# Performance work log

Hardware: AMD Instinct MI355X
Metric: run time of the kernel (lower is better)

## Reference

```python
import jax, jax.numpy as jnp
import numpy as np

N = 50257   # vocab size
D = 128     # embedding_dim
B = 2048    # batch
C = 10      # context window size


def setup_inputs() -> dict:
    key = jax.random.key(0)
    ks = jax.random.split(key, 16)
    s = 0.02
    return {
        "x_batch": jax.random.randint(ks[0], (B,), 0, N),
        "context_words_batch": jax.random.randint(ks[1], (B, C), 0, N),
        "eps": jax.random.normal(ks[2], (B, D), dtype=jnp.float32),
        # learned parameters
        "inf_emb": jax.random.normal(ks[3], (N, D), dtype=jnp.float32) * s,
        "W_aff": jax.random.normal(ks[4], (D, 2 * D), dtype=jnp.float32) * s,
        "b_aff": jnp.zeros((D,), dtype=jnp.float32),
        "W_mu": jax.random.normal(ks[5], (D, D), dtype=jnp.float32) * s,
        "b_mu": jnp.zeros((D,), dtype=jnp.float32),
        "W_sig": jax.random.normal(ks[6], (D, D), dtype=jnp.float32) * s,
        "b_sig": jnp.zeros((D,), dtype=jnp.float32),
        "gen_sigma_emb": jax.random.normal(ks[7], (N, D), dtype=jnp.float32) * s,
        "W_gen": jax.random.normal(ks[8], (N, D), dtype=jnp.float32) * s,
        "b_gen": jnp.zeros((N,), dtype=jnp.float32),
    }


def reference(x_batch, context_words_batch, eps, inf_emb, W_aff, b_aff,
              W_mu, b_mu, W_sig, b_sig, gen_sigma_emb, W_gen, b_gen):
    # ---- inference network (vectorized over batch and context) ----
    center = inf_emb[x_batch]                    # [B, D]
    ctx = inf_emb[context_words_batch]           # [B, C, D]
    center_rep = jnp.broadcast_to(center[:, None, :], ctx.shape)  # [B, C, D]
    cat = jnp.concatenate([center_rep, ctx], axis=-1)             # [B, C, 2D]
    h = jax.nn.relu(jnp.einsum("bce,de->bcd", cat, W_aff) + b_aff)
    h_sum = h.sum(axis=1)                        # [B, D]
    inf_mu = h_sum @ W_mu.T + b_mu               # [B, D]
    inf_sigma = jax.nn.softplus(h_sum @ W_sig.T + b_sig)

    # ---- reparameterized sample ----
    z = inf_mu + eps * inf_sigma                 # [B, D]

    # ---- generative / reconstruction term ----
    logits = z @ W_gen.T + b_gen                 # [B, N] (dominant intermediate)
    logp = jax.nn.log_softmax(logits, axis=-1)
    recon = jnp.take_along_axis(logp, context_words_batch, axis=1).sum(-1)  # [B]

    # ---- KL term (faithful to original, incl. use of generative sigma) ----
    sigma = jax.nn.softplus(gen_sigma_emb[x_batch])  # [B, D]
    kl = (jnp.log(sigma / inf_sigma)
          + (inf_sigma ** 2 + (inf_mu - sigma) ** 2) / (2.0 * sigma ** 2)
          - 0.5).sum(-1)                        # [B]

    return (kl - recon).mean()
```

## Files before the change

### kernel.cpp

```cpp
#include <hip/hip_runtime.h>
#include <float.h>
#include <math.h>

#define NV 50257
#define D 128
#define B 2048
#define C 10

#define NVPAD 50272
#define NTILES (NVPAD / 16)
#define NSTREAM 128
#define NG4 (NVPAD * D / 4)
#define LOG2E 1.44269504088896f
#define SC1 0x7F7F7F7F

typedef __attribute__((ext_vector_type(8))) short short8;
typedef __attribute__((ext_vector_type(8))) int int8v;
typedef __attribute__((ext_vector_type(4))) float float4v;
typedef __attribute__((ext_vector_type(2))) float float2v;

__device__ __forceinline__ float softplus_f(float x) {
    return fmaxf(x, 0.f) + log1pf(expf(-fabsf(x)));
}

__device__ __forceinline__ short f2bf(float f) {
    unsigned u = __float_as_uint(f);
    unsigned r = (u + 0x7FFFu + ((u >> 16) & 1u)) >> 16;
    return (short)r;
}

__global__ __launch_bounds__(256) void k_pre(
    const float* __restrict__ waff, const float* __restrict__ wmu,
    const float* __restrict__ wsig, const float* __restrict__ b_gen,
    short* __restrict__ waff_o, short* __restrict__ wmu_o,
    short* __restrict__ wsig_o, float* __restrict__ bg2, float* __restrict__ out)
{
    const int j = blockIdx.x * 256 + threadIdx.x;
    if (j == 0) out[0] = 0.f;
    if (j < 16384) {
        const float4* src; short4* dst; int jj;
        if (j < 8192)       { src = (const float4*)waff; dst = (short4*)waff_o; jj = j; }
        else if (j < 12288) { src = (const float4*)wmu;  dst = (short4*)wmu_o;  jj = j - 8192; }
        else                { src = (const float4*)wsig; dst = (short4*)wsig_o; jj = j - 12288; }
        const float4 g = src[jj];
        short4 o;
        o.x = f2bf(g.x); o.y = f2bf(g.y); o.z = f2bf(g.z); o.w = f2bf(g.w);
        dst[jj] = o;
    } else {
        const int jj = j - 16384;
        if (jj < NVPAD / 4) {
            const int e0 = jj * 4;
            float4 o;
            o.x = (e0 + 0 < NV) ? b_gen[e0 + 0] * LOG2E : -INFINITY;
            o.y = (e0 + 1 < NV) ? b_gen[e0 + 1] * LOG2E : -INFINITY;
            o.z = (e0 + 2 < NV) ? b_gen[e0 + 2] * LOG2E : -INFINITY;
            o.w = (e0 + 3 < NV) ? b_gen[e0 + 3] * LOG2E : -INFINITY;
            ((float4*)bg2)[jj] = o;
        }
    }
}

#define CONVB 629
__global__ __launch_bounds__(640, 1) void k_main(
    const int* __restrict__ x_batch, const int* __restrict__ ctxw,
    const float* __restrict__ eps, const float* __restrict__ inf_emb,
    const short* __restrict__ waff_bf, const float* __restrict__ b_aff,
    const short* __restrict__ wmu_bf, const float* __restrict__ b_mu,
    const short* __restrict__ wsig_bf, const float* __restrict__ b_sig,
    const float* __restrict__ gen_sig_emb, const float* __restrict__ wg,
    unsigned char* __restrict__ w8,
    float* __restrict__ z_out, unsigned char* __restrict__ z8_out,
    float* __restrict__ kl_out)
{
    const int bid = blockIdx.x;
    const int t = threadIdx.x;

    __shared__ float us[16][132];
    __shared__ float hsp[5][16][132];
    __shared__ float kl_s[8][16];

    if (bid >= 128) {
        const int base = (bid - 128) * (640 * 4) + t;
        #pragma unroll
        for (int k = 0; k < 4; ++k) {
            const int i4 = base + k * 640;
            if (i4 < NG4) {
                const int e0 = i4 * 4;
                int pk = 0;
                if (e0 < NV * D) {
                    const float4 g = ((const float4*)wg)[i4];
                    pk = __builtin_amdgcn_cvt_pk_fp8_f32(g.x, g.y, 0, false);
                    pk = __builtin_amdgcn_cvt_pk_fp8_f32(g.z, g.w, pk, true);
                }
                ((int*)w8)[i4] = pk;
            }
        }
        return;
    }

    const int b0 = bid * 16;
    const int wv = t >> 6;
    const int lane = t & 63;
    const int col16 = lane & 15;
    const int quad = lane >> 4;
    const int brow = b0 + col16;

    const int widx = ctxw[brow * C + wv];
    short8 cx[4];
    #pragma unroll
    for (int ks = 0; ks < 4; ++ks) {
        const float* p = inf_emb + (size_t)widx * D + ks * 32 + quad * 8;
        const float4 g0 = *(const float4*)p;
        const float4 g1 = *(const float4*)(p + 4);
        short8 v;
        v[0] = f2bf(g0.x); v[1] = f2bf(g0.y); v[2] = f2bf(g0.z); v[3] = f2bf(g0.w);
        v[4] = f2bf(g1.x); v[5] = f2bf(g1.y); v[6] = f2bf(g1.z); v[7] = f2bf(g1.w);
        cx[ks] = v;
    }

    if (wv < 8) {
        const int cidx = x_batch[brow];
        short8 ce[4];
        #pragma unroll
        for (int ks = 0; ks < 4; ++ks) {
            const float* p = inf_emb + (size_t)cidx * D + ks * 32 + quad * 8;
            const float4 g0 = *(const float4*)p;
            const float4 g1 = *(const float4*)(p + 4);
            short8 v;
            v[0] = f2bf(g0.x); v[1] = f2bf(g0.y); v[2] = f2bf(g0.z); v[3] = f2bf(g0.w);
            v[4] = f2bf(g1.x); v[5] = f2bf(g1.y); v[6] = f2bf(g1.z); v[7] = f2bf(g1.w);
            ce[ks] = v;
        }
        float4v acc = {0.f, 0.f, 0.f, 0.f};
        #pragma unroll
        for (int ks = 0; ks < 4; ++ks) {
            const short8 bw = *(const short8*)(waff_bf + (wv * 16 + col16) * 256 + ks * 32 + quad * 8);
            acc = __builtin_amdgcn_mfma_f32_16x16x32_bf16(ce[ks], bw, acc, 0, 0, 0);
        }
        #pragma unroll
        for (int r = 0; r < 4; ++r)
            us[quad * 4 + r][wv * 16 + col16] = acc[r];
    }
    __syncthreads();

    float ba[8];
    #pragma unroll
    for (int dt = 0; dt < 8; ++dt) ba[dt] = b_aff[dt * 16 + col16];

    float4v H[8];
    #pragma unroll
    for (int dt = 0; dt < 8; ++dt) {
        float4v a = {0.f, 0.f, 0.f, 0.f};
        #pragma unroll
        for (int ks = 0; ks < 4; ++ks) {
            const short8 bw = *(const short8*)(waff_bf + (dt * 16 + col16) * 256 + 128 + ks * 32 + quad * 8);
            a = __builtin_amdgcn_mfma_f32_16x16x32_bf16(cx[ks], bw, a, 0, 0, 0);
        }
        #pragma unroll
        for (int r = 0; r < 4; ++r) {
            const float u = us[quad * 4 + r][dt * 16 + col16];
            H[dt][r] = fmaxf(u + a[r] + ba[dt], 0.f);
        }
    }

    if (wv < 5) {
        #pragma unroll
        for (int dt = 0; dt < 8; ++dt)
            #pragma unroll
            for (int r = 0; r < 4; ++r)
                hsp[wv][quad * 4 + r][dt * 16 + col16] = H[dt][r];
    }
    __syncthreads();
    if (wv >= 5) {
        #pragma unroll
        for (int dt = 0; dt < 8; ++dt)
            #pragma unroll
            for (int r = 0; r < 4; ++r)
                hsp[wv - 5][quad * 4 + r][dt * 16 + col16] += H[dt][r];
    }
    __syncthreads();

    if (wv < 8) {
        short8 ha[4];
        #pragma unroll
        for (int ks = 0; ks < 4; ++ks) {
            const int off = ks * 32 + quad * 8;
            float4 s0 = {0.f, 0.f, 0.f, 0.f}, s1 = {0.f, 0.f, 0.f, 0.f};
            #pragma unroll
            for (int w = 0; w < 5; ++w) {
                const float4 a0 = *(const float4*)&hsp[w][col16][off];
                const float4 a1 = *(const float4*)&hsp[w][col16][off + 4];
                s0.x += a0.x; s0.y += a0.y; s0.z += a0.z; s0.w += a0.w;
                s1.x += a1.x; s1.y += a1.y; s1.z += a1.z; s1.w += a1.w;
            }
            short8 v;
            v[0] = f2bf(s0.x); v[1] = f2bf(s0.y); v[2] = f2bf(s0.z); v[3] = f2bf(s0.w);
            v[4] = f2bf(s1.x); v[5] = f2bf(s1.y); v[6] = f2bf(s1.z); v[7] = f2bf(s1.w);
            ha[ks] = v;
        }

        int xb2[4];
        #pragma unroll
        for (int r = 0; r < 4; ++r) xb2[r] = x_batch[b0 + quad * 4 + r];

        const int nt = wv;
        float4v mu4 = {0.f, 0.f, 0.f, 0.f};
        float4v sg4 = {0.f, 0.f, 0.f, 0.f};
        #pragma unroll
        for (int ks = 0; ks < 4; ++ks) {
            const short8 bm = *(const short8*)(wmu_bf + (nt * 16 + col16) * 128 + ks * 32 + quad * 8);
            const short8 bs = *(const short8*)(wsig_bf + (nt * 16 + col16) * 128 + ks * 32 + quad * 8);
            mu4 = __builtin_amdgcn_mfma_f32_16x16x32_bf16(ha[ks], bm, mu4, 0, 0, 0);
            sg4 = __builtin_amdgcn_mfma_f32_16x16x32_bf16(ha[ks], bs, sg4, 0, 0, 0);
        }
        const int d = nt * 16 + col16;
        const float bmu = b_mu[d];
        const float bsg = b_sig[d];
        float klp[4];
        #pragma unroll
        for (int r = 0; r < 4; ++r) {
            const int b = b0 + quad * 4 + r;
            const float mu = mu4[r] + bmu;
            const float sg = sg4[r] + bsg;
            const float isig = softplus_f(sg);
            const float e = eps[b * D + d];
            const float zz = fmaf(e, isig, mu);
            z_out[b * D + d] = zz;
            const int pk = __builtin_amdgcn_cvt_pk_fp8_f32(zz * LOG2E, 0.f, 0, false);
            z8_out[b * D + d] = (unsigned char)(pk & 0xFF);
            const float gs = softplus_f(gen_sig_emb[(size_t)xb2[r] * D + d]);
            const float diff = mu - gs;
            klp[r] = logf(gs / isig) + (isig * isig + diff * diff) / (2.f * gs * gs) - 0.5f;
        }
        #pragma unroll
        for (int off = 1; off < 16; off <<= 1)
            #pragma unroll
            for (int r = 0; r < 4; ++r)
                klp[r] += __shfl_xor(klp[r], off, 64);
        if (col16 == 0) {
            #pragma unroll
            for (int r = 0; r < 4; ++r)
                kl_s[wv][quad * 4 + r] = klp[r];
        }
    }
    __syncthreads();
    if (t < 16) {
        float s = 0.f;
        #pragma unroll
        for (int w = 0; w < 8; ++w) s += kl_s[w][t];
        kl_out[b0 + t] = s;
    }
}

#define LOADT8(bf, g, T) { \
    const int v_ = (T) < NTILES; \
    const int tt_ = v_ ? (T) : 0; \
    bf = *(const int8v*)(w8 + (size_t)(tt_ * 16 + col16) * D + quad * 32); \
    g = v_ ? bg2t[tt_ * 16 + col16] : -INFINITY; }

#define COMP8(bf, g) { \
    _Pragma("unroll") \
    for (int rt = 0; rt < 4; ++rt) { \
        float4v c = {g, g, g, g}; \
        c = __builtin_amdgcn_mfma_scale_f32_16x16x128_f8f6f4( \
                afrag[rt], bf, c, 0, 0, 0, SC1, 0, SC1); \
        _Pragma("unroll") \
        for (int r = 0; r < 4; ++r) \
            sums[rt][r] += __builtin_amdgcn_exp2f(c[r]); \
    } }

__global__ __launch_bounds__(256) void k_lse_mfma(
    const unsigned char* __restrict__ z8, const unsigned char* __restrict__ w8,
    const float* __restrict__ bg2t, float* __restrict__ part_s)
{
    const int bid = blockIdx.x;
    const int s = bid & 127;
    const int x = bid >> 7;
    const int t = threadIdx.x;
    const int wv = t >> 6;
    const int lane = t & 63;
    const int col16 = lane & 15;
    const int quad = lane >> 4;
    const int rowbase = x * 256 + wv * 64;

    int8v afrag[4];
    #pragma unroll
    for (int rt = 0; rt < 4; ++rt)
        afrag[rt] = *(const int8v*)(z8 + (size_t)(rowbase + rt * 16 + col16) * D + quad * 32);

    float sums[4][4];
    #pragma unroll
    for (int rt = 0; rt < 4; ++rt)
        #pragma unroll
        for (int r = 0; r < 4; ++r) sums[rt][r] = 0.f;

    int8v bA, bB, bC, bD;
    float gA, gB, gC, gD;
    LOADT8(bA, gA, s);
    LOADT8(bB, gB, s + 128);
    LOADT8(bC, gC, s + 256);
    LOADT8(bD, gD, s + 384);
    #pragma unroll 1
    for (int j = 0; j < 20; j += 4) {
        COMP8(bA, gA); LOADT8(bA, gA, s + (j + 4) * 128);
        COMP8(bB, gB); LOADT8(bB, gB, s + (j + 5) * 128);
        COMP8(bC, gC); LOADT8(bC, gC, s + (j + 6) * 128);
        COMP8(bD, gD); LOADT8(bD, gD, s + (j + 7) * 128);
    }
    COMP8(bA, gA);
    COMP8(bB, gB); COMP8(bC, gC); COMP8(bD, gD);
    LOADT8(bA, gA, s + 24 * 128);
    COMP8(bA, gA);

    #pragma unroll
    for (int off = 1; off < 16; off <<= 1)
        #pragma unroll
        for (int rt = 0; rt < 4; ++rt)
            #pragma unroll
            for (int r = 0; r < 4; ++r)
                sums[rt][r] += __shfl_xor(sums[rt][r], off, 64);

    if (col16 == 0) {
        #pragma unroll
        for (int rt = 0; rt < 4; ++rt)
            #pragma unroll
            for (int r = 0; r < 4; ++r) {
                const int row = rowbase + rt * 16 + quad * 4 + r;
                part_s[row * NSTREAM + s] = sums[rt][r];
            }
    }
}

__global__ __launch_bounds__(256) void k_final(
    const float* __restrict__ z, const unsigned char* __restrict__ w8,
    const float* __restrict__ b_gen, const int* __restrict__ ctxw,
    const float* __restrict__ part_s, const float* __restrict__ kl,
    float* __restrict__ out)
{
    const int t = threadIdx.x;
    const int wv = t >> 6;
    const int lane = t & 63;
    __shared__ float red[4];

    float wsum = 0.f;
    #pragma unroll
    for (int rr = 0; rr < 2; ++rr) {
        const int b = blockIdx.x * 8 + wv * 2 + rr;

        int idxs[C];
        #pragma unroll
        for (int c = 0; c < C; ++c) idxs[c] = ctxw[b * C + c];
        unsigned short uw[C];
        #pragma unroll
        for (int c = 0; c < C; ++c)
            uw[c] = *(const unsigned short*)(w8 + (size_t)idxs[c] * D + lane * 2);
        float sum_bg = 0.f;
        #pragma unroll
        for (int c = 0; c < C; ++c) sum_bg += b_gen[idxs[c]];

        float sv = part_s[b * NSTREAM + lane] + part_s[b * NSTREAM + 64 + lane];
        const float z0 = z[b * D + lane * 2];
        const float z1 = z[b * D + lane * 2 + 1];

        float acc = 0.f;
        #pragma unroll
        for (int c = 0; c < C; ++c) {
            const float2v wf = __builtin_amdgcn_cvt_pk_f32_fp8((int)uw[c], false);
            acc = fmaf(z0, wf[0], acc);
            acc = fmaf(z1, wf[1], acc);
        }
        #pragma unroll
        for (int off = 32; off > 0; off >>= 1) {
            sv  += __shfl_xor(sv, off, 64);
            acc += __shfl_xor(acc, off, 64);
        }
        if (lane == 0) {
            const float lse = logf(sv);
            const float recon = acc + sum_bg - C * lse;
            wsum += kl[b] - recon;
        }
    }
    if (lane == 0) red[wv] = wsum;
    __syncthreads();
    if (t == 0) atomicAdd(out, (red[0] + red[1] + red[2] + red[3]) * (1.f / B));
}

extern "C" void kernel_launch(void* const* d_in, const int* in_sizes, int n_in,
                              void* d_out, int out_size, void* d_ws, size_t ws_size,
                              hipStream_t stream) {
    const int* x_batch = (const int*)d_in[0];
    const int* ctxw    = (const int*)d_in[1];
    const float* eps   = (const float*)d_in[2];
    const float* inf_emb = (const float*)d_in[3];
    const float* W_aff = (const float*)d_in[4];
    const float* b_aff = (const float*)d_in[5];
    const float* W_mu  = (const float*)d_in[6];
    const float* b_mu  = (const float*)d_in[7];
    const float* W_sig = (const float*)d_in[8];
    const float* b_sig = (const float*)d_in[9];
    const float* gen_sig = (const float*)d_in[10];
    const float* W_gen = (const float*)d_in[11];
    const float* b_gen = (const float*)d_in[12];
    float* out = (float*)d_out;

    char* ws = (char*)d_ws;
    float* z      = (float*)ws;   ws += (size_t)B * D * 4;
    float* part_s = (float*)ws;   ws += (size_t)B * NSTREAM * 4;
    float* kl     = (float*)ws;   ws += (size_t)B * 4;
    float* bg2    = (float*)ws;   ws += (size_t)NVPAD * 4;
    unsigned char* z8 = (unsigned char*)ws;  ws += (size_t)B * D;
    unsigned char* w8 = (unsigned char*)ws;  ws += (size_t)NVPAD * D;
    short* waff_bf = (short*)ws;  ws += (size_t)128 * 256 * 2;
    short* wmu_bf  = (short*)ws;  ws += (size_t)128 * 128 * 2;
    short* wsig_bf = (short*)ws;  ws += (size_t)128 * 128 * 2;

    const int pre_items = 16384 + NVPAD / 4;
    hipLaunchKernelGGL(k_pre, dim3((pre_items + 255) / 256), dim3(256), 0, stream,
                       W_aff, W_mu, W_sig, b_gen,
                       waff_bf, wmu_bf, wsig_bf, bg2, out);
    hipLaunchKernelGGL(k_main, dim3(128 + CONVB), dim3(640), 0, stream,
                       x_batch, ctxw, eps, inf_emb, waff_bf, b_aff, wmu_bf, b_mu,
                       wsig_bf, b_sig, gen_sig, W_gen, w8, z, z8, kl);
    hipLaunchKernelGGL(k_lse_mfma, dim3(8 * NSTREAM), dim3(256), 0, stream,
                       z8, w8, bg2, part_s);
    hipLaunchKernelGGL(k_final, dim3(B / 8), dim3(256), 0, stream,
                       z, w8, b_gen, ctxw, part_s, kl, out);
}
```

Measured before the change: 177.5 us.

## Move W_gen FP8 conversion into pre-kernel and prefetch eps/gen_sigma loads

```diff
diff --git a/kernel.cpp b/kernel.cpp
--- a/kernel.cpp
+++ b/kernel.cpp
@@ -29,13 +29,39 @@
     return (short)r;
 }
 
+#define PRE_B 114
+#define CONVB8 786
 __global__ __launch_bounds__(256) void k_pre(
     const float* __restrict__ waff, const float* __restrict__ wmu,
     const float* __restrict__ wsig, const float* __restrict__ b_gen,
+    const float* __restrict__ wg,
     short* __restrict__ waff_o, short* __restrict__ wmu_o,
-    short* __restrict__ wsig_o, float* __restrict__ bg2, float* __restrict__ out)
+    short* __restrict__ wsig_o, float* __restrict__ bg2,
+    unsigned char* __restrict__ w8, float* __restrict__ out)
 {
-    const int j = blockIdx.x * 256 + threadIdx.x;
+    const int bid = blockIdx.x;
+    const int t = threadIdx.x;
+
+    if (bid >= PRE_B) {
+        const int base = (bid - PRE_B) * (256 * 8) + t;
+        #pragma unroll
+        for (int k = 0; k < 8; ++k) {
+            const int i4 = base + k * 256;
+            if (i4 < NG4) {
+                const int e0 = i4 * 4;
+                int pk = 0;
+                if (e0 < NV * D) {
+                    const float4 g = ((const float4*)wg)[i4];
+                    pk = __builtin_amdgcn_cvt_pk_fp8_f32(g.x, g.y, 0, false);
+                    pk = __builtin_amdgcn_cvt_pk_fp8_f32(g.z, g.w, pk, true);
+                }
+                ((int*)w8)[i4] = pk;
+            }
+        }
+        return;
+    }
+
+    const int j = bid * 256 + t;
     if (j == 0) out[0] = 0.f;
     if (j < 16384) {
         const float4* src; short4* dst; int jj;
@@ -60,15 +86,13 @@
     }
 }
 
-#define CONVB 629
 __global__ __launch_bounds__(640, 1) void k_main(
     const int* __restrict__ x_batch, const int* __restrict__ ctxw,
     const float* __restrict__ eps, const float* __restrict__ inf_emb,
     const short* __restrict__ waff_bf, const float* __restrict__ b_aff,
     const short* __restrict__ wmu_bf, const float* __restrict__ b_mu,
     const short* __restrict__ wsig_bf, const float* __restrict__ b_sig,
-    const float* __restrict__ gen_sig_emb, const float* __restrict__ wg,
-    unsigned char* __restrict__ w8,
+    const float* __restrict__ gen_sig_emb,
     float* __restrict__ z_out, unsigned char* __restrict__ z8_out,
     float* __restrict__ kl_out)
 {
@@ -78,25 +102,6 @@
     __shared__ float us[16][132];
     __shared__ float hsp[5][16][132];
     __shared__ float kl_s[8][16];
-
-    if (bid >= 128) {
-        const int base = (bid - 128) * (640 * 4) + t;
-        #pragma unroll
-        for (int k = 0; k < 4; ++k) {
-            const int i4 = base + k * 640;
-            if (i4 < NG4) {
-                const int e0 = i4 * 4;
-                int pk = 0;
-                if (e0 < NV * D) {
-                    const float4 g = ((const float4*)wg)[i4];
-                    pk = __builtin_amdgcn_cvt_pk_fp8_f32(g.x, g.y, 0, false);
-                    pk = __builtin_amdgcn_cvt_pk_fp8_f32(g.z, g.w, pk, true);
-                }
-                ((int*)w8)[i4] = pk;
-            }
-        }
-        return;
-    }
 
     const int b0 = bid * 16;
     const int wv = t >> 6;
@@ -116,6 +121,19 @@
         v[0] = f2bf(g0.x); v[1] = f2bf(g0.y); v[2] = f2bf(g0.z); v[3] = f2bf(g0.w);
         v[4] = f2bf(g1.x); v[5] = f2bf(g1.y); v[6] = f2bf(g1.z); v[7] = f2bf(g1.w);
         cx[ks] = v;
+    }
+
+    int xb2[4];
+    float gsr[4], epr[4];
+    const int dd = wv * 16 + col16;
+    if (wv < 8) {
+        #pragma unroll
+        for (int r = 0; r < 4; ++r) xb2[r] = x_batch[b0 + quad * 4 + r];
+        #pragma unroll
+        for (int r = 0; r < 4; ++r) {
+            gsr[r] = gen_sig_emb[(size_t)xb2[r] * D + dd];
+            epr[r] = eps[(b0 + quad * 4 + r) * D + dd];
+        }
     }
 
     if (wv < 8) {
@@ -199,10 +217,6 @@
             ha[ks] = v;
         }
 
-        int xb2[4];
-        #pragma unroll
-        for (int r = 0; r < 4; ++r) xb2[r] = x_batch[b0 + quad * 4 + r];
-
         const int nt = wv;
         float4v mu4 = {0.f, 0.f, 0.f, 0.f};
         float4v sg4 = {0.f, 0.f, 0.f, 0.f};
@@ -223,12 +237,12 @@
             const float mu = mu4[r] + bmu;
             const float sg = sg4[r] + bsg;
             const float isig = softplus_f(sg);
-            const float e = eps[b * D + d];
+            const float e = epr[r];
             const float zz = fmaf(e, isig, mu);
             z_out[b * D + d] = zz;
             const int pk = __builtin_amdgcn_cvt_pk_fp8_f32(zz * LOG2E, 0.f, 0, false);
             z8_out[b * D + d] = (unsigned char)(pk & 0xFF);
-            const float gs = softplus_f(gen_sig_emb[(size_t)xb2[r] * D + d]);
+            const float gs = softplus_f(gsr[r]);
             const float diff = mu - gs;
             klp[r] = logf(gs / isig) + (isig * isig + diff * diff) / (2.f * gs * gs) - 0.5f;
         }
@@ -414,13 +428,12 @@
     short* wmu_bf  = (short*)ws;  ws += (size_t)128 * 128 * 2;
     short* wsig_bf = (short*)ws;  ws += (size_t)128 * 128 * 2;
 
-    const int pre_items = 16384 + NVPAD / 4;
-    hipLaunchKernelGGL(k_pre, dim3((pre_items + 255) / 256), dim3(256), 0, stream,
-                       W_aff, W_mu, W_sig, b_gen,
-                       waff_bf, wmu_bf, wsig_bf, bg2, out);
-    hipLaunchKernelGGL(k_main, dim3(128 + CONVB), dim3(640), 0, stream,
+    hipLaunchKernelGGL(k_pre, dim3(PRE_B + CONVB8), dim3(256), 0, stream,
+                       W_aff, W_mu, W_sig, b_gen, W_gen,
+                       waff_bf, wmu_bf, wsig_bf, bg2, w8, out);
+    hipLaunchKernelGGL(k_main, dim3(128), dim3(640), 0, stream,
                        x_batch, ctxw, eps, inf_emb, waff_bf, b_aff, wmu_bf, b_mu,
-                       wsig_bf, b_sig, gen_sig, W_gen, w8, z, z8, kl);
+                       wsig_bf, b_sig, gen_sig, z, z8, kl);
     hipLaunchKernelGGL(k_lse_mfma, dim3(8 * NSTREAM), dim3(256), 0, stream,
                        z8, w8, bg2, part_s);
     hipLaunchKernelGGL(k_final, dim3(B / 8), dim3(256), 0, stream,
```

Result: slower. 182.1 us (+2.6%).

## Fuse all stages into one cooperative persistent kernel with grid syncs

Applied to the files above, without the earlier changes.

```diff
diff --git a/kernel.cpp b/kernel.cpp
--- a/kernel.cpp
+++ b/kernel.cpp
@@ -1,6 +1,9 @@
 #include <hip/hip_runtime.h>
+#include <hip/hip_cooperative_groups.h>
 #include <float.h>
 #include <math.h>
+
+namespace cg = cooperative_groups;
 
 #define NV 50257
 #define D 128
@@ -14,6 +17,9 @@
 #define LOG2E 1.44269504088896f
 #define SC1 0x7F7F7F7F
 
+#define MEGAB 512
+#define INFB 256
+
 typedef __attribute__((ext_vector_type(8))) short short8;
 typedef __attribute__((ext_vector_type(8))) int int8v;
 typedef __attribute__((ext_vector_type(4))) float float4v;
@@ -27,6 +33,369 @@
     unsigned u = __float_as_uint(f);
     unsigned r = (u + 0x7FFFu + ((u >> 16) & 1u)) >> 16;
     return (short)r;
+}
+
+#define LOADEMB(dst, idx) { \
+    const float* p_ = inf_emb + (size_t)(idx) * D; \
+    _Pragma("unroll") \
+    for (int ks_ = 0; ks_ < 4; ++ks_) { \
+        const float4 g0_ = *(const float4*)(p_ + ks_ * 32 + quad * 8); \
+        const float4 g1_ = *(const float4*)(p_ + ks_ * 32 + quad * 8 + 4); \
+        short8 v_; \
+        v_[0] = f2bf(g0_.x); v_[1] = f2bf(g0_.y); v_[2] = f2bf(g0_.z); v_[3] = f2bf(g0_.w); \
+        v_[4] = f2bf(g1_.x); v_[5] = f2bf(g1_.y); v_[6] = f2bf(g1_.z); v_[7] = f2bf(g1_.w); \
+        dst[ks_] = v_; } }
+
+#define ACCUM_H(cxf) { \
+    _Pragma("unroll") \
+    for (int dt_ = 0; dt_ < 8; ++dt_) { \
+        float4v a_ = {0.f, 0.f, 0.f, 0.f}; \
+        _Pragma("unroll") \
+        for (int ks_ = 0; ks_ < 4; ++ks_) { \
+            const short8 bw_ = *(const short8*)(waff_bf + (dt_ * 16 + col16) * 256 + 128 + ks_ * 32 + quad * 8); \
+            a_ = __builtin_amdgcn_mfma_f32_16x16x32_bf16(cxf[ks_], bw_, a_, 0, 0, 0); } \
+        _Pragma("unroll") \
+        for (int r_ = 0; r_ < 4; ++r_) { \
+            const float u_ = us[quad * 4 + r_][dt_ * 16 + col16]; \
+            H[dt_][r_] += fmaxf(u_ + a_[r_] + ba[dt_], 0.f); } } }
+
+#define LOADT8(bf, g, T) { \
+    const int v_ = (T) < NTILES; \
+    const int tt_ = v_ ? (T) : 0; \
+    bf = *(const int8v*)(w8 + (size_t)(tt_ * 16 + col16) * D + quad * 32); \
+    g = v_ ? bg2[tt_ * 16 + col16] : -INFINITY; }
+
+#define COMP8(bf, g) { \
+    _Pragma("unroll") \
+    for (int rt = 0; rt < 4; ++rt) { \
+        float4v c = {g, g, g, g}; \
+        c = __builtin_amdgcn_mfma_scale_f32_16x16x128_f8f6f4( \
+                afrag[rt], bf, c, 0, 0, 0, SC1, 0, SC1); \
+        _Pragma("unroll") \
+        for (int r = 0; r < 4; ++r) \
+            sums[rt][r] += __builtin_amdgcn_exp2f(c[r]); \
+    } }
+
+__global__ __launch_bounds__(256, 2) void k_mega(
+    const int* __restrict__ x_batch, const int* __restrict__ ctxw,
+    const float* __restrict__ eps, const float* __restrict__ inf_emb,
+    const float* __restrict__ W_aff, const float* __restrict__ b_aff,
+    const float* __restrict__ W_mu, const float* __restrict__ b_mu,
+    const float* __restrict__ W_sig, const float* __restrict__ b_sig,
+    const float* __restrict__ gen_sig_emb, const float* __restrict__ wg,
+    const float* __restrict__ b_gen,
+    short* __restrict__ waff_bf, short* __restrict__ wmu_bf, short* __restrict__ wsig_bf,
+    float* __restrict__ bg2, unsigned char* __restrict__ w8,
+    float* __restrict__ z_out, unsigned char* __restrict__ z8_out,
+    float* __restrict__ kl_out, float* __restrict__ part_s,
+    float* __restrict__ out)
+{
+    cg::grid_group grid = cg::this_grid();
+    const int bid = blockIdx.x;
+    const int t = threadIdx.x;
+    const int wv = t >> 6;
+    const int lane = t & 63;
+    const int col16 = lane & 15;
+    const int quad = lane >> 4;
+
+    __shared__ float us[16][132];
+    __shared__ float hsp[2][16][132];
+    __shared__ float kl_s[4][8];
+    __shared__ float red[4];
+
+    if (bid >= INFB) {
+        const int j = (bid - INFB) * 256 + t;
+        if (j == 0) out[0] = 0.f;
+        if (j < 16384) {
+            const float4* src; short4* dst; int jj;
+            if (j < 8192)       { src = (const float4*)W_aff; dst = (short4*)waff_bf; jj = j; }
+            else if (j < 12288) { src = (const float4*)W_mu;  dst = (short4*)wmu_bf;  jj = j - 8192; }
+            else                { src = (const float4*)W_sig; dst = (short4*)wsig_bf; jj = j - 12288; }
+            const float4 g = src[jj];
+            short4 o;
+            o.x = f2bf(g.x); o.y = f2bf(g.y); o.z = f2bf(g.z); o.w = f2bf(g.w);
+            dst[jj] = o;
+        } else {
+            const int jj = j - 16384;
+            if (jj < NVPAD / 4) {
+                const int e0 = jj * 4;
+                float4 o;
+                o.x = (e0 + 0 < NV) ? b_gen[e0 + 0] * LOG2E : -INFINITY;
+                o.y = (e0 + 1 < NV) ? b_gen[e0 + 1] * LOG2E : -INFINITY;
+                o.z = (e0 + 2 < NV) ? b_gen[e0 + 2] * LOG2E : -INFINITY;
+                o.w = (e0 + 3 < NV) ? b_gen[e0 + 3] * LOG2E : -INFINITY;
+                ((float4*)bg2)[jj] = o;
+            }
+        }
+    }
+    grid.sync();
+
+    if (bid < INFB) {
+        const int b0 = bid * 8;
+        const int brow = b0 + (col16 & 7);
+
+        const int nc = (wv < 2) ? 3 : 2;
+        const int wi0 = ctxw[brow * C + wv];
+        const int wi1 = ctxw[brow * C + wv + 4];
+        const int wi2 = (wv < 2) ? ctxw[brow * C + 8 + wv] : 0;
+        const int cidx = x_batch[brow];
+
+        short8 ce[4], cxa[4], cxb[4];
+        LOADEMB(ce, cidx);
+        LOADEMB(cxa, wi0);
+
+        float4v u0 = {0.f, 0.f, 0.f, 0.f}, u1 = {0.f, 0.f, 0.f, 0.f};
+        #pragma unroll
+        for (int ks = 0; ks < 4; ++ks) {
+            const short8 bw0 = *(const short8*)(waff_bf + ((wv    ) * 16 + col16) * 256 + ks * 32 + quad * 8);
+            const short8 bw1 = *(const short8*)(waff_bf + ((wv + 4) * 16 + col16) * 256 + ks * 32 + quad * 8);
+            u0 = __builtin_amdgcn_mfma_f32_16x16x32_bf16(ce[ks], bw0, u0, 0, 0, 0);
+            u1 = __builtin_amdgcn_mfma_f32_16x16x32_bf16(ce[ks], bw1, u1, 0, 0, 0);
+        }
+        #pragma unroll
+        for (int r = 0; r < 4; ++r) {
+            us[quad * 4 + r][(wv    ) * 16 + col16] = u0[r];
+            us[quad * 4 + r][(wv + 4) * 16 + col16] = u1[r];
+        }
+        __syncthreads();
+
+        float ba[8];
+        #pragma unroll
+        for (int dt = 0; dt < 8; ++dt) ba[dt] = b_aff[dt * 16 + col16];
+
+        float4v H[8];
+        #pragma unroll
+        for (int dt = 0; dt < 8; ++dt) H[dt] = (float4v){0.f, 0.f, 0.f, 0.f};
+
+        LOADEMB(cxb, wi1);
+        ACCUM_H(cxa);
+        if (nc == 3) {
+            LOADEMB(cxa, wi2);
+            ACCUM_H(cxb);
+            ACCUM_H(cxa);
+        } else {
+            ACCUM_H(cxb);
+        }
+
+        if (wv < 2) {
+            #pragma unroll
+            for (int dt = 0; dt < 8; ++dt)
+                #pragma unroll
+                for (int r = 0; r < 4; ++r)
+                    hsp[wv][quad * 4 + r][dt * 16 + col16] = H[dt][r];
+        }
+        __syncthreads();
+        if (wv >= 2) {
+            #pragma unroll
+            for (int dt = 0; dt < 8; ++dt)
+                #pragma unroll
+                for (int r = 0; r < 4; ++r)
+                    hsp[wv - 2][quad * 4 + r][dt * 16 + col16] += H[dt][r];
+        }
+        __syncthreads();
+
+        short8 ha[4];
+        #pragma unroll
+        for (int ks = 0; ks < 4; ++ks) {
+            const int off = ks * 32 + quad * 8;
+            const float4 a0 = *(const float4*)&hsp[0][col16][off];
+            const float4 b0v = *(const float4*)&hsp[1][col16][off];
+            const float4 a1 = *(const float4*)&hsp[0][col16][off + 4];
+            const float4 b1v = *(const float4*)&hsp[1][col16][off + 4];
+            short8 v;
+            v[0] = f2bf(a0.x + b0v.x); v[1] = f2bf(a0.y + b0v.y);
+            v[2] = f2bf(a0.z + b0v.z); v[3] = f2bf(a0.w + b0v.w);
+            v[4] = f2bf(a1.x + b1v.x); v[5] = f2bf(a1.y + b1v.y);
+            v[6] = f2bf(a1.z + b1v.z); v[7] = f2bf(a1.w + b1v.w);
+            ha[ks] = v;
+        }
+
+        const int d0 = wv * 16 + col16;
+        const int d1 = (wv + 4) * 16 + col16;
+        int xb2[4]; float gs0[4], gs1[4], ep0[4], ep1[4];
+        #pragma unroll
+        for (int r = 0; r < 4; ++r) {
+            const int br = b0 + ((quad * 4 + r) & 7);
+            xb2[r] = x_batch[br];
+            gs0[r] = gen_sig_emb[(size_t)xb2[r] * D + d0];
+            gs1[r] = gen_sig_emb[(size_t)xb2[r] * D + d1];
+            ep0[r] = eps[br * D + d0];
+            ep1[r] = eps[br * D + d1];
+        }
+
+        float4v mu0 = {0.f,0.f,0.f,0.f}, sg0v = {0.f,0.f,0.f,0.f};
+        float4v mu1 = {0.f,0.f,0.f,0.f}, sg1v = {0.f,0.f,0.f,0.f};
+        #pragma unroll
+        for (int ks = 0; ks < 4; ++ks) {
+            const short8 bm0 = *(const short8*)(wmu_bf  + ((wv    ) * 16 + col16) * 128 + ks * 32 + quad * 8);
+            const short8 bs0 = *(const short8*)(wsig_bf + ((wv    ) * 16 + col16) * 128 + ks * 32 + quad * 8);
+            const short8 bm1 = *(const short8*)(wmu_bf  + ((wv + 4) * 16 + col16) * 128 + ks * 32 + quad * 8);
+            const short8 bs1 = *(const short8*)(wsig_bf + ((wv + 4) * 16 + col16) * 128 + ks * 32 + quad * 8);
+            mu0  = __builtin_amdgcn_mfma_f32_16x16x32_bf16(ha[ks], bm0, mu0, 0, 0, 0);
+            sg0v = __builtin_amdgcn_mfma_f32_16x16x32_bf16(ha[ks], bs0, sg0v, 0, 0, 0);
+            mu1  = __builtin_amdgcn_mfma_f32_16x16x32_bf16(ha[ks], bm1, mu1, 0, 0, 0);
+            sg1v = __builtin_amdgcn_mfma_f32_16x16x32_bf16(ha[ks], bs1, sg1v, 0, 0, 0);
+        }
+
+        float klp[4] = {0.f, 0.f, 0.f, 0.f};
+        #pragma unroll
+        for (int half = 0; half < 2; ++half) {
+            const int d = half ? d1 : d0;
+            const float bmu = b_mu[d];
+            const float bsg = b_sig[d];
+            #pragma unroll
+            for (int r = 0; r < 4; ++r) {
+                const int b = b0 + quad * 4 + r;
+                const float mu = (half ? mu1[r] : mu0[r]) + bmu;
+                const float sg = (half ? sg1v[r] : sg0v[r]) + bsg;
+                const float isig = softplus_f(sg);
+                const float e = half ? ep1[r] : ep0[r];
+                const float zz = fmaf(e, isig, mu);
+                if (quad < 2) {
+                    z_out[b * D + d] = zz;
+                    const int pk = __builtin_amdgcn_cvt_pk_fp8_f32(zz * LOG2E, 0.f, 0, false);
+                    z8_out[b * D + d] = (unsigned char)(pk & 0xFF);
+                }
+                const float gs = softplus_f(half ? gs1[r] : gs0[r]);
+                const float diff = mu - gs;
+                klp[r] += logf(gs / isig) + (isig * isig + diff * diff) / (2.f * gs * gs) - 0.5f;
+            }
+        }
+        #pragma unroll
+        for (int off = 1; off < 16; off <<= 1)
+            #pragma unroll
+            for (int r = 0; r < 4; ++r)
+                klp[r] += __shfl_xor(klp[r], off, 64);
+        if (col16 == 0 && quad < 2) {
+            #pragma unroll
+            for (int r = 0; r < 4; ++r)
+                kl_s[wv][quad * 4 + r] = klp[r];
+        }
+        __syncthreads();
+        if (t < 8) {
+            float s = 0.f;
+            #pragma unroll
+            for (int w = 0; w < 4; ++w) s += kl_s[w][t];
+            kl_out[b0 + t] = s;
+        }
+    } else {
+        const int base = (bid - INFB) * 256 + t;
+        #pragma unroll 5
+        for (int k = 0; k < 25; ++k) {
+            const int i4 = base + k * 65536;
+            if (i4 < NG4) {
+                const int e0 = i4 * 4;
+                int pk = 0;
+                if (e0 < NV * D) {
+                    const float4 g = ((const float4*)wg)[i4];
+                    pk = __builtin_amdgcn_cvt_pk_fp8_f32(g.x, g.y, 0, false);
+                    pk = __builtin_amdgcn_cvt_pk_fp8_f32(g.z, g.w, pk, true);
+                }
+                ((int*)w8)[i4] = pk;
+            }
+        }
+    }
+    grid.sync();
+
+    #pragma unroll 1
+    for (int rep = 0; rep < 2; ++rep) {
+        const int gwid = bid * 4 + wv + rep * 2048;
+        const int s = gwid & 127;
+        const int x = gwid >> 7;
+        const int rowbase = x * 64;
+
+        int8v afrag[4];
+        #pragma unroll
+        for (int rt = 0; rt < 4; ++rt)
+            afrag[rt] = *(const int8v*)(z8_out + (size_t)(rowbase + rt * 16 + col16) * D + quad * 32);
+
+        float sums[4][4];
+        #pragma unroll
+        for (int rt = 0; rt < 4; ++rt)
+            #pragma unroll
+            for (int r = 0; r < 4; ++r) sums[rt][r] = 0.f;
+
+        int8v bA, bB, bC, bD;
+        float gA, gB, gC, gD;
+        LOADT8(bA, gA, s);
+        LOADT8(bB, gB, s + 128);
+        LOADT8(bC, gC, s + 256);
+        LOADT8(bD, gD, s + 384);
+        #pragma unroll 1
+        for (int j = 0; j < 20; j += 4) {
+            COMP8(bA, gA); LOADT8(bA, gA, s + (j + 4) * 128);
+            COMP8(bB, gB); LOADT8(bB, gB, s + (j + 5) * 128);
+            COMP8(bC, gC); LOADT8(bC, gC, s + (j + 6) * 128);
+            COMP8(bD, gD); LOADT8(bD, gD, s + (j + 7) * 128);
+        }
+        COMP8(bA, gA);
+        COMP8(bB, gB); COMP8(bC, gC); COMP8(bD, gD);
+        LOADT8(bA, gA, s + 24 * 128);
+        COMP8(bA, gA);
+
+        #pragma unroll
+        for (int off = 1; off < 16; off <<= 1)
+            #pragma unroll
+            for (int rt = 0; rt < 4; ++rt)
+                #pragma unroll
+                for (int r = 0; r < 4; ++r)
+                    sums[rt][r] += __shfl_xor(sums[rt][r], off, 64);
+
+        if (col16 == 0) {
+            #pragma unroll
+            for (int rt = 0; rt < 4; ++rt)
+                #pragma unroll
+                for (int r = 0; r < 4; ++r) {
+                    const int row = rowbase + rt * 16 + quad * 4 + r;
+                    part_s[row * NSTREAM + s] = sums[rt][r];
+                }
+        }
+    }
+    grid.sync();
+
+    if (bid < INFB) {
+        float wsum = 0.f;
+        #pragma unroll
+        for (int rr = 0; rr < 2; ++rr) {
+            const int b = bid * 8 + wv * 2 + rr;
+
+            int idxs[C];
+            #pragma unroll
+            for (int c = 0; c < C; ++c) idxs[c] = ctxw[b * C + c];
+            unsigned short uw[C];
+            #pragma unroll
+            for (int c = 0; c < C; ++c)
+                uw[c] = *(const unsigned short*)(w8 + (size_t)idxs[c] * D + lane * 2);
+            float sum_bg = 0.f;
+            #pragma unroll
+            for (int c = 0; c < C; ++c) sum_bg += b_gen[idxs[c]];
+
+            float sv = part_s[b * NSTREAM + lane] + part_s[b * NSTREAM + 64 + lane];
+            const float z0 = z_out[b * D + lane * 2];
+            const float z1 = z_out[b * D + lane * 2 + 1];
+
+            float acc = 0.f;
+            #pragma unroll
+            for (int c = 0; c < C; ++c) {
+                const float2v wf = __builtin_amdgcn_cvt_pk_f32_fp8((int)uw[c], false);
+                acc = fmaf(z0, wf[0], acc);
+                acc = fmaf(z1, wf[1], acc);
+            }
+            #pragma unroll
+            for (int off = 32; off > 0; off >>= 1) {
+                sv  += __shfl_xor(sv, off, 64);
+                acc += __shfl_xor(acc, off, 64);
+            }
+            if (lane == 0) {
+                const float lse = logf(sv);
+                const float recon = acc + sum_bg - C * lse;
+                wsum += kl_out[b] - recon;
+            }
+        }
+        if (lane == 0) red[wv] = wsum;
+        __syncthreads();
+        if (t == 0) atomicAdd(out, (red[0] + red[1] + red[2] + red[3]) * (1.f / B));
+    }
 }
 
 __global__ __launch_bounds__(256) void k_pre(
@@ -107,30 +476,12 @@
 
     const int widx = ctxw[brow * C + wv];
     short8 cx[4];
-    #pragma unroll
-    for (int ks = 0; ks < 4; ++ks) {
-        const float* p = inf_emb + (size_t)widx * D + ks * 32 + quad * 8;
-        const float4 g0 = *(const float4*)p;
-        const float4 g1 = *(const float4*)(p + 4);
-        short8 v;
-        v[0] = f2bf(g0.x); v[1] = f2bf(g0.y); v[2] = f2bf(g0.z); v[3] = f2bf(g0.w);
-        v[4] = f2bf(g1.x); v[5] = f2bf(g1.y); v[6] = f2bf(g1.z); v[7] = f2bf(g1.w);
-        cx[ks] = v;
-    }
+    LOADEMB(cx, widx);
 
     if (wv < 8) {
         const int cidx = x_batch[brow];
         short8 ce[4];
-        #pragma unroll
-        for (int ks = 0; ks < 4; ++ks) {
-            const float* p = inf_emb + (size_t)cidx * D + ks * 32 + quad * 8;
-            const float4 g0 = *(const float4*)p;
-            const float4 g1 = *(const float4*)(p + 4);
-            short8 v;
-            v[0] = f2bf(g0.x); v[1] = f2bf(g0.y); v[2] = f2bf(g0.z); v[3] = f2bf(g0.w);
-            v[4] = f2bf(g1.x); v[5] = f2bf(g1.y); v[6] = f2bf(g1.z); v[7] = f2bf(g1.w);
-            ce[ks] = v;
-        }
+        LOADEMB(ce, cidx);
         float4v acc = {0.f, 0.f, 0.f, 0.f};
         #pragma unroll
         for (int ks = 0; ks < 4; ++ks) {
@@ -252,26 +603,9 @@
     }
 }
 
-#define LOADT8(bf, g, T) { \
-    const int v_ = (T) < NTILES; \
-    const int tt_ = v_ ? (T) : 0; \
-    bf = *(const int8v*)(w8 + (size_t)(tt_ * 16 + col16) * D + quad * 32); \
-    g = v_ ? bg2t[tt_ * 16 + col16] : -INFINITY; }
-
-#define COMP8(bf, g) { \
-    _Pragma("unroll") \
-    for (int rt = 0; rt < 4; ++rt) { \
-        float4v c = {g, g, g, g}; \
-        c = __builtin_amdgcn_mfma_scale_f32_16x16x128_f8f6f4( \
-                afrag[rt], bf, c, 0, 0, 0, SC1, 0, SC1); \
-        _Pragma("unroll") \
-        for (int r = 0; r < 4; ++r) \
-            sums[rt][r] += __builtin_amdgcn_exp2f(c[r]); \
-    } }
-
 __global__ __launch_bounds__(256) void k_lse_mfma(
     const unsigned char* __restrict__ z8, const unsigned char* __restrict__ w8,
-    const float* __restrict__ bg2t, float* __restrict__ part_s)
+    const float* __restrict__ bg2, float* __restrict__ part_s)
 {
     const int bid = blockIdx.x;
     const int s = bid & 127;
@@ -414,15 +748,28 @@
     short* wmu_bf  = (short*)ws;  ws += (size_t)128 * 128 * 2;
     short* wsig_bf = (short*)ws;  ws += (size_t)128 * 128 * 2;
 
-    const int pre_items = 16384 + NVPAD / 4;
-    hipLaunchKernelGGL(k_pre, dim3((pre_items + 255) / 256), dim3(256), 0, stream,
-                       W_aff, W_mu, W_sig, b_gen,
-                       waff_bf, wmu_bf, wsig_bf, bg2, out);
-    hipLaunchKernelGGL(k_main, dim3(128 + CONVB), dim3(640), 0, stream,
-                       x_batch, ctxw, eps, inf_emb, waff_bf, b_aff, wmu_bf, b_mu,
-                       wsig_bf, b_sig, gen_sig, W_gen, w8, z, z8, kl);
-    hipLaunchKernelGGL(k_lse_mfma, dim3(8 * NSTREAM), dim3(256), 0, stream,
-                       z8, w8, bg2, part_s);
-    hipLaunchKernelGGL(k_final, dim3(B / 8), dim3(256), 0, stream,
-                       z, w8, b_gen, ctxw, part_s, kl, out);
+    void* kargs[] = {
+        (void*)&x_batch, (void*)&ctxw, (void*)&eps, (void*)&inf_emb,
+        (void*)&W_aff, (void*)&b_aff, (void*)&W_mu, (void*)&b_mu,
+        (void*)&W_sig, (void*)&b_sig, (void*)&gen_sig, (void*)&W_gen, (void*)&b_gen,
+        (void*)&waff_bf, (void*)&wmu_bf, (void*)&wsig_bf,
+        (void*)&bg2, (void*)&w8, (void*)&z, (void*)&z8, (void*)&kl, (void*)&part_s,
+        (void*)&out
+    };
+    hipError_t err = hipLaunchCooperativeKernel((const void*)k_mega, dim3(MEGAB), dim3(256),
+                                                kargs, 0, stream);
+    if (err != hipSuccess) {
+        (void)hipGetLastError();
+        const int pre_items = 16384 + NVPAD / 4;
+        hipLaunchKernelGGL(k_pre, dim3((pre_items + 255) / 256), dim3(256), 0, stream,
+                           W_aff, W_mu, W_sig, b_gen,
+                           waff_bf, wmu_bf, wsig_bf, bg2, out);
+        hipLaunchKernelGGL(k_main, dim3(128 + CONVB), dim3(640), 0, stream,
+                           x_batch, ctxw, eps, inf_emb, waff_bf, b_aff, wmu_bf, b_mu,
+                           wsig_bf, b_sig, gen_sig, W_gen, w8, z, z8, kl);
+        hipLaunchKernelGGL(k_lse_mfma, dim3(8 * NSTREAM), dim3(256), 0, stream,
+                           z8, w8, bg2, part_s);
+        hipLaunchKernelGGL(k_final, dim3(B / 8), dim3(256), 0, stream,
+                           z, w8, b_gen, ctxw, part_s, kl, out);
+    }
 }
```

Measured after the change: 370.6 us. 109% more time.

## Drop pre-kernel by converting weights inline and staging embedding gathers in LDS

Applied to the files above, without the earlier changes.

```diff
diff --git a/kernel.cpp b/kernel.cpp
--- a/kernel.cpp
+++ b/kernel.cpp
@@ -29,54 +29,36 @@
     return (short)r;
 }
 
-__global__ __launch_bounds__(256) void k_pre(
-    const float* __restrict__ waff, const float* __restrict__ wmu,
-    const float* __restrict__ wsig, const float* __restrict__ b_gen,
-    short* __restrict__ waff_o, short* __restrict__ wmu_o,
-    short* __restrict__ wsig_o, float* __restrict__ bg2, float* __restrict__ out)
-{
-    const int j = blockIdx.x * 256 + threadIdx.x;
-    if (j == 0) out[0] = 0.f;
-    if (j < 16384) {
-        const float4* src; short4* dst; int jj;
-        if (j < 8192)       { src = (const float4*)waff; dst = (short4*)waff_o; jj = j; }
-        else if (j < 12288) { src = (const float4*)wmu;  dst = (short4*)wmu_o;  jj = j - 8192; }
-        else                { src = (const float4*)wsig; dst = (short4*)wsig_o; jj = j - 12288; }
-        const float4 g = src[jj];
-        short4 o;
-        o.x = f2bf(g.x); o.y = f2bf(g.y); o.z = f2bf(g.z); o.w = f2bf(g.w);
-        dst[jj] = o;
-    } else {
-        const int jj = j - 16384;
-        if (jj < NVPAD / 4) {
-            const int e0 = jj * 4;
-            float4 o;
-            o.x = (e0 + 0 < NV) ? b_gen[e0 + 0] * LOG2E : -INFINITY;
-            o.y = (e0 + 1 < NV) ? b_gen[e0 + 1] * LOG2E : -INFINITY;
-            o.z = (e0 + 2 < NV) ? b_gen[e0 + 2] * LOG2E : -INFINITY;
-            o.w = (e0 + 3 < NV) ? b_gen[e0 + 3] * LOG2E : -INFINITY;
-            ((float4*)bg2)[jj] = o;
-        }
-    }
-}
+#define LOADW8(dst, base_ptr) { \
+    const float4 w0_ = *(const float4*)(base_ptr); \
+    const float4 w1_ = *(const float4*)((base_ptr) + 4); \
+    short8 v_; \
+    v_[0] = f2bf(w0_.x); v_[1] = f2bf(w0_.y); v_[2] = f2bf(w0_.z); v_[3] = f2bf(w0_.w); \
+    v_[4] = f2bf(w1_.x); v_[5] = f2bf(w1_.y); v_[6] = f2bf(w1_.z); v_[7] = f2bf(w1_.w); \
+    dst = v_; }
 
 #define CONVB 629
 __global__ __launch_bounds__(640, 1) void k_main(
     const int* __restrict__ x_batch, const int* __restrict__ ctxw,
     const float* __restrict__ eps, const float* __restrict__ inf_emb,
-    const short* __restrict__ waff_bf, const float* __restrict__ b_aff,
-    const short* __restrict__ wmu_bf, const float* __restrict__ b_mu,
-    const short* __restrict__ wsig_bf, const float* __restrict__ b_sig,
+    const float* __restrict__ W_aff, const float* __restrict__ b_aff,
+    const float* __restrict__ W_mu, const float* __restrict__ b_mu,
+    const float* __restrict__ W_sig, const float* __restrict__ b_sig,
     const float* __restrict__ gen_sig_emb, const float* __restrict__ wg,
-    unsigned char* __restrict__ w8,
+    const float* __restrict__ b_gen,
+    unsigned char* __restrict__ w8, float* __restrict__ bg2,
     float* __restrict__ z_out, unsigned char* __restrict__ z8_out,
     float* __restrict__ kl_out)
 {
     const int bid = blockIdx.x;
     const int t = threadIdx.x;
 
+    __shared__ union {
+        float hsp[5][16][132];
+        unsigned short rows[176][136];
+    } u;
+    __shared__ int idx_s[176];
     __shared__ float us[16][132];
-    __shared__ float hsp[5][16][132];
     __shared__ float kl_s[8][16];
 
     if (bid >= 128) {
@@ -95,6 +77,16 @@
                 ((int*)w8)[i4] = pk;
             }
         }
+        const int jb = (bid - 128) * 640 + t;
+        if (jb < NVPAD / 4) {
+            const int e0 = jb * 4;
+            float4 o;
+            o.x = (e0 + 0 < NV) ? b_gen[e0 + 0] * LOG2E : -INFINITY;
+            o.y = (e0 + 1 < NV) ? b_gen[e0 + 1] * LOG2E : -INFINITY;
+            o.z = (e0 + 2 < NV) ? b_gen[e0 + 2] * LOG2E : -INFINITY;
+            o.w = (e0 + 3 < NV) ? b_gen[e0 + 3] * LOG2E : -INFINITY;
+            ((float4*)bg2)[jb] = o;
+        }
         return;
     }
 
@@ -103,38 +95,38 @@
     const int lane = t & 63;
     const int col16 = lane & 15;
     const int quad = lane >> 4;
-    const int brow = b0 + col16;
-
-    const int widx = ctxw[brow * C + wv];
+
+    if (t < 160) {
+        idx_s[16 + (t % 10) * 16 + (t / 10)] = ctxw[b0 * C + t];
+    } else if (t < 176) {
+        idx_s[t - 160] = x_batch[b0 + (t - 160)];
+    }
+    __syncthreads();
+
+    for (int s = wv; s < 176; s += 10) {
+        const float2 g = ((const float2*)(inf_emb + (size_t)idx_s[s] * D))[lane];
+        ushort2 o;
+        o.x = (unsigned short)f2bf(g.x);
+        o.y = (unsigned short)f2bf(g.y);
+        *(ushort2*)&u.rows[s][lane * 2] = o;
+    }
+    __syncthreads();
+
     short8 cx[4];
     #pragma unroll
-    for (int ks = 0; ks < 4; ++ks) {
-        const float* p = inf_emb + (size_t)widx * D + ks * 32 + quad * 8;
-        const float4 g0 = *(const float4*)p;
-        const float4 g1 = *(const float4*)(p + 4);
-        short8 v;
-        v[0] = f2bf(g0.x); v[1] = f2bf(g0.y); v[2] = f2bf(g0.z); v[3] = f2bf(g0.w);
-        v[4] = f2bf(g1.x); v[5] = f2bf(g1.y); v[6] = f2bf(g1.z); v[7] = f2bf(g1.w);
-        cx[ks] = v;
-    }
+    for (int ks = 0; ks < 4; ++ks)
+        cx[ks] = *(const short8*)&u.rows[16 + wv * 16 + col16][ks * 32 + quad * 8];
 
     if (wv < 8) {
-        const int cidx = x_batch[brow];
         short8 ce[4];
         #pragma unroll
+        for (int ks = 0; ks < 4; ++ks)
+            ce[ks] = *(const short8*)&u.rows[col16][ks * 32 + quad * 8];
+        float4v acc = {0.f, 0.f, 0.f, 0.f};
+        #pragma unroll
         for (int ks = 0; ks < 4; ++ks) {
-            const float* p = inf_emb + (size_t)cidx * D + ks * 32 + quad * 8;
-            const float4 g0 = *(const float4*)p;
-            const float4 g1 = *(const float4*)(p + 4);
-            short8 v;
-            v[0] = f2bf(g0.x); v[1] = f2bf(g0.y); v[2] = f2bf(g0.z); v[3] = f2bf(g0.w);
-            v[4] = f2bf(g1.x); v[5] = f2bf(g1.y); v[6] = f2bf(g1.z); v[7] = f2bf(g1.w);
-            ce[ks] = v;
-        }
-        float4v acc = {0.f, 0.f, 0.f, 0.f};
-        #pragma unroll
-        for (int ks = 0; ks < 4; ++ks) {
-            const short8 bw = *(const short8*)(waff_bf + (wv * 16 + col16) * 256 + ks * 32 + quad * 8);
+            short8 bw;
+            LOADW8(bw, W_aff + (wv * 16 + col16) * 256 + ks * 32 + quad * 8);
             acc = __builtin_amdgcn_mfma_f32_16x16x32_bf16(ce[ks], bw, acc, 0, 0, 0);
         }
         #pragma unroll
@@ -153,13 +145,14 @@
         float4v a = {0.f, 0.f, 0.f, 0.f};
         #pragma unroll
         for (int ks = 0; ks < 4; ++ks) {
-            const short8 bw = *(const short8*)(waff_bf + (dt * 16 + col16) * 256 + 128 + ks * 32 + quad * 8);
+            short8 bw;
+            LOADW8(bw, W_aff + (dt * 16 + col16) * 256 + 128 + ks * 32 + quad * 8);
             a = __builtin_amdgcn_mfma_f32_16x16x32_bf16(cx[ks], bw, a, 0, 0, 0);
         }
         #pragma unroll
         for (int r = 0; r < 4; ++r) {
-            const float u = us[quad * 4 + r][dt * 16 + col16];
-            H[dt][r] = fmaxf(u + a[r] + ba[dt], 0.f);
+            const float uu = us[quad * 4 + r][dt * 16 + col16];
+            H[dt][r] = fmaxf(uu + a[r] + ba[dt], 0.f);
         }
     }
 
@@ -168,7 +161,7 @@
         for (int dt = 0; dt < 8; ++dt)
             #pragma unroll
             for (int r = 0; r < 4; ++r)
-                hsp[wv][quad * 4 + r][dt * 16 + col16] = H[dt][r];
+                u.hsp[wv][quad * 4 + r][dt * 16 + col16] = H[dt][r];
     }
     __syncthreads();
     if (wv >= 5) {
@@ -176,7 +169,7 @@
         for (int dt = 0; dt < 8; ++dt)
             #pragma unroll
             for (int r = 0; r < 4; ++r)
-                hsp[wv - 5][quad * 4 + r][dt * 16 + col16] += H[dt][r];
+                u.hsp[wv - 5][quad * 4 + r][dt * 16 + col16] += H[dt][r];
     }
     __syncthreads();
 
@@ -188,8 +181,8 @@
             float4 s0 = {0.f, 0.f, 0.f, 0.f}, s1 = {0.f, 0.f, 0.f, 0.f};
             #pragma unroll
             for (int w = 0; w < 5; ++w) {
-                const float4 a0 = *(const float4*)&hsp[w][col16][off];
-                const float4 a1 = *(const float4*)&hsp[w][col16][off + 4];
+                const float4 a0 = *(const float4*)&u.hsp[w][col16][off];
+                const float4 a1 = *(const float4*)&u.hsp[w][col16][off + 4];
                 s0.x += a0.x; s0.y += a0.y; s0.z += a0.z; s0.w += a0.w;
                 s1.x += a1.x; s1.y += a1.y; s1.z += a1.z; s1.w += a1.w;
             }
@@ -208,8 +201,9 @@
         float4v sg4 = {0.f, 0.f, 0.f, 0.f};
         #pragma unroll
         for (int ks = 0; ks < 4; ++ks) {
-            const short8 bm = *(const short8*)(wmu_bf + (nt * 16 + col16) * 128 + ks * 32 + quad * 8);
-            const short8 bs = *(const short8*)(wsig_bf + (nt * 16 + col16) * 128 + ks * 32 + quad * 8);
+            short8 bm, bs;
+            LOADW8(bm, W_mu  + (nt * 16 + col16) * 128 + ks * 32 + quad * 8);
+            LOADW8(bs, W_sig + (nt * 16 + col16) * 128 + ks * 32 + quad * 8);
             mu4 = __builtin_amdgcn_mfma_f32_16x16x32_bf16(ha[ks], bm, mu4, 0, 0, 0);
             sg4 = __builtin_amdgcn_mfma_f32_16x16x32_bf16(ha[ks], bs, sg4, 0, 0, 0);
         }
@@ -271,9 +265,11 @@
 
 __global__ __launch_bounds__(256) void k_lse_mfma(
     const unsigned char* __restrict__ z8, const unsigned char* __restrict__ w8,
-    const float* __restrict__ bg2t, float* __restrict__ part_s)
+    const float* __restrict__ bg2t, float* __restrict__ part_s,
+    float* __restrict__ out)
 {
     const int bid = blockIdx.x;
+    if (bid == 0 && threadIdx.x == 0) out[0] = 0.f;
     const int s = bid & 127;
     const int x = bid >> 7;
     const int t = threadIdx.x;
@@ -410,19 +406,12 @@
     float* bg2    = (float*)ws;   ws += (size_t)NVPAD * 4;
     unsigned char* z8 = (unsigned char*)ws;  ws += (size_t)B * D;
     unsigned char* w8 = (unsigned char*)ws;  ws += (size_t)NVPAD * D;
-    short* waff_bf = (short*)ws;  ws += (size_t)128 * 256 * 2;
-    short* wmu_bf  = (short*)ws;  ws += (size_t)128 * 128 * 2;
-    short* wsig_bf = (short*)ws;  ws += (size_t)128 * 128 * 2;
-
-    const int pre_items = 16384 + NVPAD / 4;
-    hipLaunchKernelGGL(k_pre, dim3((pre_items + 255) / 256), dim3(256), 0, stream,
-                       W_aff, W_mu, W_sig, b_gen,
-                       waff_bf, wmu_bf, wsig_bf, bg2, out);
+
     hipLaunchKernelGGL(k_main, dim3(128 + CONVB), dim3(640), 0, stream,
-                       x_batch, ctxw, eps, inf_emb, waff_bf, b_aff, wmu_bf, b_mu,
-                       wsig_bf, b_sig, gen_sig, W_gen, w8, z, z8, kl);
+                       x_batch, ctxw, eps, inf_emb, W_aff, b_aff, W_mu, b_mu,
+                       W_sig, b_sig, gen_sig, W_gen, b_gen, w8, bg2, z, z8, kl);
     hipLaunchKernelGGL(k_lse_mfma, dim3(8 * NSTREAM), dim3(256), 0, stream,
-                       z8, w8, bg2, part_s);
+                       z8, w8, bg2, part_s, out);
     hipLaunchKernelGGL(k_final, dim3(B / 8), dim3(256), 0, stream,
                        z, w8, b_gen, ctxw, part_s, kl, out);
 }
```

New measurement: 189.1 us. +6.5%, slower.
